# Optimization experiments

Hardware: AMD Instinct MI355X
Metric: run time of the kernel (lower is better)

Reference implementation:

```python
import jax, jax.numpy as jnp
import numpy as np

R, S, D_IN, WIDTH, K = 8192, 128, 16, 64, 8  # rays, samples/ray, feat dim, net_width, net_kernels


def setup_inputs() -> dict:
    key = jax.random.key(0)
    ks = jax.random.split(key, 8)
    he = jax.nn.initializers.he_uniform()
    idxs = jax.random.randint(ks[0], (R, S), 0, K, dtype=jnp.int32)
    xs = jax.random.normal(ks[1], (R, S, D_IN), dtype=jnp.float32)
    # MultiMLP params: net_depth=2 hidden MultiDense layers + 1 output layer, each with K kernels
    W0 = he(ks[2], (K, D_IN, WIDTH), jnp.float32)
    b0 = jnp.zeros((K, WIDTH), jnp.float32)
    W1 = he(ks[3], (K, WIDTH, WIDTH), jnp.float32)
    b1 = jnp.zeros((K, WIDTH), jnp.float32)
    W2 = he(ks[4], (K, WIDTH, 1), jnp.float32)
    b2 = jnp.zeros((K, 1), jnp.float32)
    return {"idxs": idxs, "xs": xs, "W0": W0, "b0": b0, "W1": W1, "b1": b1, "W2": W2, "b2": b2}


def _multi_dense(idx, x, W, b):
    """Per-sample kernel select: out[n] = x[n] @ W[idx[n]] + b[idx[n]].

    x: [N, d], W: [K, d, f], b: [K, f], idx: [N] int. Loop is over the small
    fixed kernel count K (not a data dim); avoids materializing an [N, d, f]
    gathered-weight tensor.
    """
    out = jnp.zeros((x.shape[0], W.shape[-1]), x.dtype)
    zero = jnp.zeros((), x.dtype)
    for k in range(W.shape[0]):
        sel = (idx == k)[:, None]
        out = out + jnp.where(sel, x @ W[k] + b[k], zero)
    return out


def reference(idxs, xs, W0, b0, W1, b1, W2, b2):
    batch_shape = idxs.shape  # (R, S)
    idx = idxs.reshape(-1)
    h = xs.reshape(-1, xs.shape[-1])
    h = jax.nn.relu(_multi_dense(idx, h, W0, b0))
    h = jax.nn.relu(_multi_dense(idx, h, W1, b1))
    out = _multi_dense(idx, h, W2, b2)  # [N, 1] density
    return out.reshape(*batch_shape, 1)
```

## Files before the change

### kernel.cpp

```cpp
#include <hip/hip_runtime.h>


typedef __attribute__((ext_vector_type(8))) short bfrag;
typedef __attribute__((ext_vector_type(4))) float ffrag;

#define SPAN        512
#define NSPANS      2048
#define IMG_STRIDE  15360
#define WS_NEED     ((size_t)(8 * IMG_STRIDE))

__device__ __forceinline__ unsigned short bf16r(float f) {
    unsigned int u = __float_as_uint(f);
    u += 0x7fffu + ((u >> 16) & 1u);
    return (unsigned short)(u >> 16);
}
__device__ __forceinline__ unsigned int pack_trunc(float hiF, float loF) {
    return __builtin_amdgcn_perm(__float_as_uint(hiF), __float_as_uint(loF), 0x07060302u);
}
__device__ __forceinline__ unsigned int pack_rnd(float hiF, float loF) {
    return __builtin_amdgcn_perm(__float_as_uint(hiF) + 0x8000u,
                                 __float_as_uint(loF) + 0x8000u, 0x07060302u);
}
__device__ __forceinline__ bfrag mkfrag(unsigned int a, unsigned int b,
                                        unsigned int c, unsigned int d) {
    union { unsigned int u[4]; bfrag f; } x;
    x.u[0] = a; x.u[1] = b; x.u[2] = c; x.u[3] = d;
    return x.f;
}

__global__ void k_build_images(const float* __restrict__ W0, const float* __restrict__ b0,
                               const float* __restrict__ W1, const float* __restrict__ b1,
                               const float* __restrict__ W2, const float* __restrict__ b2,
                               unsigned char* __restrict__ wsB) {
    const int k = blockIdx.x, t = threadIdx.x;
    unsigned char* img = wsB + k * IMG_STRIDE;
    unsigned short* w0a = (unsigned short*)img;
    unsigned short* w1a = (unsigned short*)(img + 4096);
    unsigned short* w2a = (unsigned short*)(img + 12288);
    float* bias = (float*)(img + 14336);
    for (int e = t; e < 2048; e += 256) {
        int j = e & 7, lane = (e >> 3) & 63, nt = e >> 9, q = lane >> 4, l15 = lane & 15;
        unsigned short v = 0;
        if (q < 2) {
            v = bf16r(W0[k * 1024 + (q * 8 + j) * 64 + nt * 16 + l15]);
        } else if (q == 2 && j < 2) {
            float b = b0[k * 64 + nt * 16 + l15];
            unsigned short hb = bf16r(b);
            if (j == 0) v = hb;
            else        v = bf16r(b - __uint_as_float((unsigned int)hb << 16));
        }
        w0a[e] = v;
    }
    for (int e = t; e < 4096; e += 256) {
        int j = e & 7, lane = (e >> 3) & 63, s = (e >> 9) & 1, nt = e >> 10;
        int q = lane >> 4, l15 = lane & 15;
        int h = s * 32 + ((j < 4) ? (q * 4 + j) : (16 + q * 4 + (j - 4)));
        w1a[e] = bf16r(W1[k * 4096 + h * 64 + nt * 16 + l15]);
    }
    for (int e = t; e < 1024; e += 256) {
        int j = e & 7, lane = (e >> 3) & 63, s = e >> 9, q = lane >> 4, l15 = lane & 15;
        int h = s * 32 + ((j < 4) ? (q * 4 + j) : (16 + q * 4 + (j - 4)));
        w2a[e] = (l15 == 0) ? bf16r(W2[k * 64 + h]) : (unsigned short)0;
    }
    if (t < 64) bias[t] = b1[k * 64 + t];
    else if (t == 64) bias[64] = b2[k];
}

__global__ __launch_bounds__(256, 4) void k_fused(const int* __restrict__ idxs,
                                                  const float* __restrict__ xs,
                                                  const unsigned char* __restrict__ wsB,
                                                  float* __restrict__ out) {
    __shared__ int wcnt[2][4][8];
    __shared__ int bsbase[2][4][8];
    __shared__ int cntS[8], startS[8];
    __shared__ unsigned short sId[SPAN];
    __shared__ __align__(16) unsigned short Xg[SPAN * 16];
    __shared__ float outBuf[SPAN];

    const int tid = threadIdx.x, lane = tid & 63, w = tid >> 6;
    const int q = lane >> 4, l15 = lane & 15;
    const int base = blockIdx.x * SPAN;

    int kreg[2], lrank[2];
    #pragma unroll
    for (int it = 0; it < 2; ++it) {
        int k = idxs[base + it * 256 + tid];
        kreg[it] = k;
        unsigned long long mymask = 0;
        #pragma unroll
        for (int kk = 0; kk < 8; ++kk) {
            unsigned long long m = __ballot(k == kk);
            if (k == kk) mymask = m;
            if (lane == 0) wcnt[it][w][kk] = (int)__popcll(m);
        }
        lrank[it] = (int)__popcll(mymask & ((1ull << lane) - 1ull));
    }
    __syncthreads();
    if (tid < 8) {
        int c = 0;
        for (int it = 0; it < 2; ++it)
            for (int w2 = 0; w2 < 4; ++w2) c += wcnt[it][w2][tid];
        cntS[tid] = c;
    }
    __syncthreads();
    if (tid == 0) {
        int s = 0;
        for (int k = 0; k < 8; ++k) { startS[k] = s; s += cntS[k]; }
    }
    __syncthreads();
    if (tid < 64) {
        int it = tid >> 5, w2 = (tid >> 3) & 3, kk = tid & 7;
        int b = startS[kk];
        for (int it2 = 0; it2 < it; ++it2)
            for (int w3 = 0; w3 < 4; ++w3) b += wcnt[it2][w3][kk];
        for (int w3 = 0; w3 < w2; ++w3) b += wcnt[it][w3][kk];
        bsbase[it][w2][kk] = b;
    }
    __syncthreads();
    #pragma unroll
    for (int it = 0; it < 2; ++it)
        sId[bsbase[it][w][kreg[it]] + lrank[it]] = (unsigned short)(it * 256 + tid);
    __syncthreads();

    #pragma unroll
    for (int it = 0; it < 2; ++it) {
        const int r = it * 256 + tid;
        const int gid = base + (int)sId[r];
        const float4* p = (const float4*)(xs + (size_t)gid * 16);
        float4 f0 = p[0], f1 = p[1], f2 = p[2], f3 = p[3];
        uint4 lo, hi;
        lo.x = pack_trunc(f0.y, f0.x); lo.y = pack_trunc(f0.w, f0.z);
        lo.z = pack_trunc(f1.y, f1.x); lo.w = pack_trunc(f1.w, f1.z);
        hi.x = pack_trunc(f2.y, f2.x); hi.y = pack_trunc(f2.w, f2.z);
        hi.z = pack_trunc(f3.y, f3.x); hi.w = pack_trunc(f3.w, f3.z);
        const int g = r >> 4, m = r & 15;
        *(uint4*)(Xg + g * 256 + m * 8)       = lo;
        *(uint4*)(Xg + g * 256 + 128 + m * 8) = hi;
    }
    __syncthreads();

    #pragma unroll
    for (int kk2 = 0; kk2 < 2; ++kk2) {
        const int k = w + kk2 * 4;
        const int cnt = cntS[k];
        if (cnt == 0) continue;
        const int start = startS[k];
        const unsigned char* img = wsB + k * IMG_STRIDE;

        bfrag w0f[4], w1f[4][2], w2f[2];
        #pragma unroll
        for (int nt = 0; nt < 4; ++nt)
            w0f[nt] = *(const bfrag*)(img + nt * 1024 + lane * 16);
        #pragma unroll
        for (int nt = 0; nt < 4; ++nt)
            #pragma unroll
            for (int s = 0; s < 2; ++s)
                w1f[nt][s] = *(const bfrag*)(img + 4096 + ((nt * 2 + s) * 64 + lane) * 16);
        #pragma unroll
        for (int s = 0; s < 2; ++s)
            w2f[s] = *(const bfrag*)(img + 12288 + (s * 64 + lane) * 16);
        const float* bias = (const float*)(img + 14336);
        ffrag b1v[4];
        #pragma unroll
        for (int nt = 0; nt < 4; ++nt)
            b1v[nt] = *(const ffrag*)(bias + nt * 16 + q * 4);
        const float b2v = bias[64];

        const int nst = (cnt + 15) >> 4;

        auto loadB = [&](int st) -> bfrag {
            int r = start + st * 16 + l15;
            int rm = start + cnt - 1;
            r = r < rm ? r : rm;
            bfrag bv = {0, 0, 0, 0, 0, 0, 0, 0};
            if (q < 2)
                bv = *(const bfrag*)(Xg + (r >> 4) * 256 + q * 128 + (r & 15) * 8);
            else if (q == 2) { bv[0] = (short)0x3F80; bv[1] = (short)0x3F80; }
            return bv;
        };

        bfrag bCur = loadB(0);
        for (int st = 0; st < nst; ++st) {
            ffrag acc0[4];
            #pragma unroll
            for (int nt = 0; nt < 4; ++nt) {
                ffrag z = {0.f, 0.f, 0.f, 0.f};
                acc0[nt] = __builtin_amdgcn_mfma_f32_16x16x32_bf16(w0f[nt], bCur, z, 0, 0, 0);
            }
            bfrag bNxt = {0, 0, 0, 0, 0, 0, 0, 0};
            if (st + 1 < nst) bNxt = loadB(st + 1);

            unsigned int P[8];
            #pragma unroll
            for (int nt = 0; nt < 4; ++nt) {
                float v0 = acc0[nt][0] > 0.f ? acc0[nt][0] : 0.f;
                float v1 = acc0[nt][1] > 0.f ? acc0[nt][1] : 0.f;
                float v2 = acc0[nt][2] > 0.f ? acc0[nt][2] : 0.f;
                float v3 = acc0[nt][3] > 0.f ? acc0[nt][3] : 0.f;
                P[nt * 2]     = pack_rnd(v1, v0);
                P[nt * 2 + 1] = pack_rnd(v3, v2);
            }
            bfrag h10 = mkfrag(P[0], P[1], P[2], P[3]);
            bfrag h11 = mkfrag(P[4], P[5], P[6], P[7]);

            ffrag acc1[4];
            #pragma unroll
            for (int nt = 0; nt < 4; ++nt) {
                acc1[nt] = __builtin_amdgcn_mfma_f32_16x16x32_bf16(w1f[nt][0], h10, b1v[nt], 0, 0, 0);
                acc1[nt] = __builtin_amdgcn_mfma_f32_16x16x32_bf16(w1f[nt][1], h11, acc1[nt], 0, 0, 0);
            }

            unsigned int Qp[8];
            #pragma unroll
            for (int nt = 0; nt < 4; ++nt) {
                float v0 = acc1[nt][0] > 0.f ? acc1[nt][0] : 0.f;
                float v1 = acc1[nt][1] > 0.f ? acc1[nt][1] : 0.f;
                float v2 = acc1[nt][2] > 0.f ? acc1[nt][2] : 0.f;
                float v3 = acc1[nt][3] > 0.f ? acc1[nt][3] : 0.f;
                Qp[nt * 2]     = pack_rnd(v1, v0);
                Qp[nt * 2 + 1] = pack_rnd(v3, v2);
            }
            bfrag h20 = mkfrag(Qp[0], Qp[1], Qp[2], Qp[3]);
            bfrag h21 = mkfrag(Qp[4], Qp[5], Qp[6], Qp[7]);

            ffrag d;
            {
                ffrag z = {0.f, 0.f, 0.f, 0.f};
                d = __builtin_amdgcn_mfma_f32_16x16x32_bf16(w2f[0], h20, z, 0, 0, 0);
                d = __builtin_amdgcn_mfma_f32_16x16x32_bf16(w2f[1], h21, d, 0, 0, 0);
            }
            if (q == 0) {
                int row = st * 16 + l15;
                if (row < cnt) outBuf[sId[start + row]] = d[0] + b2v;
            }
            bCur = bNxt;
        }
    }
    __syncthreads();

    ((float2*)(out + base))[tid] = ((const float2*)outBuf)[tid];
}

__global__ void k_fallback(const int* __restrict__ idxs, const float* __restrict__ xs,
                           const float* __restrict__ W0, const float* __restrict__ b0,
                           const float* __restrict__ W1, const float* __restrict__ b1,
                           const float* __restrict__ W2, const float* __restrict__ b2,
                           float* __restrict__ out, int N) {
    int n = blockIdx.x * blockDim.x + threadIdx.x;
    if (n >= N) return;
    int k = idxs[n];
    float h0[64];
    #pragma unroll
    for (int j = 0; j < 64; ++j) h0[j] = b0[k * 64 + j];
    for (int i = 0; i < 16; ++i) {
        float xi = xs[(size_t)n * 16 + i];
        #pragma unroll
        for (int j = 0; j < 64; ++j) h0[j] = fmaf(xi, W0[k * 1024 + i * 64 + j], h0[j]);
    }
    #pragma unroll
    for (int j = 0; j < 64; ++j) h0[j] = fmaxf(h0[j], 0.f);
    float acc = b2[k];
    for (int jc = 0; jc < 4; ++jc) {
        float h1[16];
        #pragma unroll
        for (int j = 0; j < 16; ++j) h1[j] = b1[k * 64 + jc * 16 + j];
        for (int i = 0; i < 64; ++i) {
            float hv = h0[i];
            #pragma unroll
            for (int j = 0; j < 16; ++j)
                h1[j] = fmaf(hv, W1[k * 4096 + i * 64 + jc * 16 + j], h1[j]);
        }
        #pragma unroll
        for (int j = 0; j < 16; ++j) acc = fmaf(fmaxf(h1[j], 0.f), W2[k * 64 + jc * 16 + j], acc);
    }
    out[n] = acc;
}

extern "C" void kernel_launch(void* const* d_in, const int* in_sizes, int n_in,
                              void* d_out, int out_size, void* d_ws, size_t ws_size,
                              hipStream_t stream) {
    const int*   idxs = (const int*)d_in[0];
    const float* xs   = (const float*)d_in[1];
    const float* W0   = (const float*)d_in[2];
    const float* b0   = (const float*)d_in[3];
    const float* W1   = (const float*)d_in[4];
    const float* b1   = (const float*)d_in[5];
    const float* W2   = (const float*)d_in[6];
    const float* b2   = (const float*)d_in[7];
    float* out = (float*)d_out;
    const int N = in_sizes[0];

    if (N != SPAN * NSPANS || ws_size < WS_NEED) {
        k_fallback<<<(N + 255) / 256, 256, 0, stream>>>(idxs, xs, W0, b0, W1, b1, W2, b2, out, N);
        return;
    }

    unsigned char* wsB = (unsigned char*)d_ws;
    k_build_images<<<8, 256, 0, stream>>>(W0, b0, W1, b1, W2, b2, wsB);
    k_fused<<<NSPANS, 256, 0, stream>>>(idxs, xs, wsB, out);
}
```

Baseline: 136.7 us.

## Interleave two independent MFMA chains per subtile and parallelize weight image build

The fused kernel's per-kernel loop now handles two 16-row subtiles per iteration as independent MLP chains, and prefetches the next pair of B fragments. The aim is to hide the dependent MFMA→ReLU→pack→MFMA latency within one wave. loadB becomes branchless: lanes with q==3 now read real data, which multiplies against zero weights, so results do not change. The weight-image build kernel is spread over 64 blocks instead of 8. In exchange, two live chains raise VGPR pressure, which could cause spills under the launch bound of 4 blocks.

```diff
diff --git a/kernel.cpp b/kernel.cpp
--- a/kernel.cpp
+++ b/kernel.cpp
@@ -32,13 +32,14 @@
                                const float* __restrict__ W1, const float* __restrict__ b1,
                                const float* __restrict__ W2, const float* __restrict__ b2,
                                unsigned char* __restrict__ wsB) {
-    const int k = blockIdx.x, t = threadIdx.x;
+    const int k = blockIdx.x >> 3, p = blockIdx.x & 7, t = threadIdx.x;
     unsigned char* img = wsB + k * IMG_STRIDE;
     unsigned short* w0a = (unsigned short*)img;
     unsigned short* w1a = (unsigned short*)(img + 4096);
     unsigned short* w2a = (unsigned short*)(img + 12288);
     float* bias = (float*)(img + 14336);
-    for (int e = t; e < 2048; e += 256) {
+    {
+        int e = p * 256 + t;
         int j = e & 7, lane = (e >> 3) & 63, nt = e >> 9, q = lane >> 4, l15 = lane & 15;
         unsigned short v = 0;
         if (q < 2) {
@@ -51,19 +52,24 @@
         }
         w0a[e] = v;
     }
-    for (int e = t; e < 4096; e += 256) {
+    #pragma unroll
+    for (int i = 0; i < 2; ++i) {
+        int e = p * 512 + i * 256 + t;
         int j = e & 7, lane = (e >> 3) & 63, s = (e >> 9) & 1, nt = e >> 10;
         int q = lane >> 4, l15 = lane & 15;
         int h = s * 32 + ((j < 4) ? (q * 4 + j) : (16 + q * 4 + (j - 4)));
         w1a[e] = bf16r(W1[k * 4096 + h * 64 + nt * 16 + l15]);
     }
-    for (int e = t; e < 1024; e += 256) {
+    if (t < 128) {
+        int e = p * 128 + t;
         int j = e & 7, lane = (e >> 3) & 63, s = e >> 9, q = lane >> 4, l15 = lane & 15;
         int h = s * 32 + ((j < 4) ? (q * 4 + j) : (16 + q * 4 + (j - 4)));
         w2a[e] = (l15 == 0) ? bf16r(W2[k * 64 + h]) : (unsigned short)0;
     }
-    if (t < 64) bias[t] = b1[k * 64 + t];
-    else if (t == 64) bias[64] = b2[k];
+    if (p == 0) {
+        if (t < 64) bias[t] = b1[k * 64 + t];
+        else if (t == 64) bias[64] = b2[k];
+    }
 }
 
 __global__ __launch_bounds__(256, 4) void k_fused(const int* __restrict__ idxs,
@@ -172,24 +178,18 @@
             int r = start + st * 16 + l15;
             int rm = start + cnt - 1;
             r = r < rm ? r : rm;
-            bfrag bv = {0, 0, 0, 0, 0, 0, 0, 0};
-            if (q < 2)
-                bv = *(const bfrag*)(Xg + (r >> 4) * 256 + q * 128 + (r & 15) * 8);
-            else if (q == 2) { bv[0] = (short)0x3F80; bv[1] = (short)0x3F80; }
+            bfrag bv = *(const bfrag*)(Xg + (r >> 4) * 256 + (q & 1) * 128 + (r & 15) * 8);
+            if (q == 2) { bv[0] = (short)0x3F80; bv[1] = (short)0x3F80; }
             return bv;
         };
 
-        bfrag bCur = loadB(0);
-        for (int st = 0; st < nst; ++st) {
+        auto chain = [&](bfrag bv) -> ffrag {
             ffrag acc0[4];
             #pragma unroll
             for (int nt = 0; nt < 4; ++nt) {
                 ffrag z = {0.f, 0.f, 0.f, 0.f};
-                acc0[nt] = __builtin_amdgcn_mfma_f32_16x16x32_bf16(w0f[nt], bCur, z, 0, 0, 0);
-            }
-            bfrag bNxt = {0, 0, 0, 0, 0, 0, 0, 0};
-            if (st + 1 < nst) bNxt = loadB(st + 1);
-
+                acc0[nt] = __builtin_amdgcn_mfma_f32_16x16x32_bf16(w0f[nt], bv, z, 0, 0, 0);
+            }
             unsigned int P[8];
             #pragma unroll
             for (int nt = 0; nt < 4; ++nt) {
@@ -202,14 +202,12 @@
             }
             bfrag h10 = mkfrag(P[0], P[1], P[2], P[3]);
             bfrag h11 = mkfrag(P[4], P[5], P[6], P[7]);
-
             ffrag acc1[4];
             #pragma unroll
             for (int nt = 0; nt < 4; ++nt) {
                 acc1[nt] = __builtin_amdgcn_mfma_f32_16x16x32_bf16(w1f[nt][0], h10, b1v[nt], 0, 0, 0);
                 acc1[nt] = __builtin_amdgcn_mfma_f32_16x16x32_bf16(w1f[nt][1], h11, acc1[nt], 0, 0, 0);
             }
-
             unsigned int Qp[8];
             #pragma unroll
             for (int nt = 0; nt < 4; ++nt) {
@@ -222,18 +220,34 @@
             }
             bfrag h20 = mkfrag(Qp[0], Qp[1], Qp[2], Qp[3]);
             bfrag h21 = mkfrag(Qp[4], Qp[5], Qp[6], Qp[7]);
-
-            ffrag d;
-            {
-                ffrag z = {0.f, 0.f, 0.f, 0.f};
-                d = __builtin_amdgcn_mfma_f32_16x16x32_bf16(w2f[0], h20, z, 0, 0, 0);
-                d = __builtin_amdgcn_mfma_f32_16x16x32_bf16(w2f[1], h21, d, 0, 0, 0);
-            }
+            ffrag z = {0.f, 0.f, 0.f, 0.f};
+            ffrag d = __builtin_amdgcn_mfma_f32_16x16x32_bf16(w2f[0], h20, z, 0, 0, 0);
+            d = __builtin_amdgcn_mfma_f32_16x16x32_bf16(w2f[1], h21, d, 0, 0, 0);
+            return d;
+        };
+
+        int st = 0;
+        bfrag bA = loadB(0);
+        bfrag bB = loadB(1);
+        for (; st + 1 < nst; st += 2) {
+            bfrag pA = loadB(st + 2);
+            bfrag pB = loadB(st + 3);
+            ffrag dA = chain(bA);
+            ffrag dB = chain(bB);
+            if (q == 0) {
+                int rowA = st * 16 + l15;
+                if (rowA < cnt) outBuf[sId[start + rowA]] = dA[0] + b2v;
+                int rowB = (st + 1) * 16 + l15;
+                if (rowB < cnt) outBuf[sId[start + rowB]] = dB[0] + b2v;
+            }
+            bA = pA; bB = pB;
+        }
+        if (st < nst) {
+            ffrag dA = chain(bA);
             if (q == 0) {
                 int row = st * 16 + l15;
-                if (row < cnt) outBuf[sId[start + row]] = d[0] + b2v;
-            }
-            bCur = bNxt;
+                if (row < cnt) outBuf[sId[start + row]] = dA[0] + b2v;
+            }
         }
     }
     __syncthreads();
@@ -296,6 +310,6 @@
     }
 
     unsigned char* wsB = (unsigned char*)d_ws;
-    k_build_images<<<8, 256, 0, stream>>>(W0, b0, W1, b1, W2, b2, wsB);
+    k_build_images<<<64, 256, 0, stream>>>(W0, b0, W1, b1, W2, b2, wsB);
     k_fused<<<NSPANS, 256, 0, stream>>>(idxs, xs, wsB, out);
 }
```

Measured after the change: 131.7 us. 3.6% less time.
